# Performance work log

Measured on AMD Instinct MI355X. Metric: run time of the kernel, lower is better.

## Reference

```python
import jax, jax.numpy as jnp
import numpy as np

NC, NPR, E, B = 200000, 100000, 500000, 200000
DIN, HID, HEADS = 16, 256, 8
D = HID // HEADS
NCOLOR, NSIZE, NGROUP = 1000, 30, 50


def setup_inputs() -> dict:
    key = jax.random.key(0)
    ks = jax.random.split(key, 24)
    g = lambda i, shape, s=0.05: jax.random.normal(ks[i], shape, jnp.float32) * s
    return dict(
        customer_x=g(0, (NC, DIN), 1.0),
        product_x=g(1, (NPR, DIN), 1.0),
        proj_cust_W=g(2, (DIN, HID)), proj_cust_b=jnp.zeros((HID,), jnp.float32),
        proj_prod_W=g(3, (DIN, HID)), proj_prod_b=jnp.zeros((HID,), jnp.float32),
        att_src_r=g(4, (HEADS, D)), att_dst_r=g(5, (HEADS, D)),
        att_src_rb=g(6, (HEADS, D)), att_dst_rb=g(7, (HEADS, D)),
        q_sem=g(8, (HID,)), k_lin_W=g(9, (HID, HID)), k_lin_b=jnp.zeros((HID,), jnp.float32),
        color_emb=g(10, (NCOLOR, 8), 1.0),
        size_emb=g(11, (NSIZE, 4), 1.0),
        group_emb=g(12, (NGROUP, 4), 1.0),
        fc1_W=g(13, (HID * 2 + 16, 128)), fc1_b=jnp.zeros((128,), jnp.float32),
        fc2_W=g(14, (128, 32)), fc2_b=jnp.zeros((32,), jnp.float32),
        fc3_W=g(15, (32, 1)), fc3_b=jnp.zeros((1,), jnp.float32),
        bn1_gamma=jnp.ones((128,), jnp.float32), bn1_beta=jnp.zeros((128,), jnp.float32),
        bn2_gamma=jnp.ones((32,), jnp.float32), bn2_beta=jnp.zeros((32,), jnp.float32),
        edge_src=jax.random.randint(ks[16], (E,), 0, NC),
        edge_dst=jax.random.randint(ks[17], (E,), 0, NPR),
        label_src=jax.random.randint(ks[18], (B,), 0, NC),
        label_dst=jax.random.randint(ks[19], (B,), 0, NPR),
        size_idx=jax.random.randint(ks[20], (B,), 0, NSIZE),
        color_idx=jax.random.randint(ks[21], (B,), 0, NCOLOR),
        group_idx=jax.random.randint(ks[22], (B,), 0, NGROUP),
    )


def _edge_softmax(logits, dst, n):
    # destination-grouped softmax over edges; logits: [E,H]
    m = jax.ops.segment_max(logits, dst, num_segments=n)
    m = jnp.where(jnp.isfinite(m), m, 0.0)
    e = jnp.exp(logits - m[dst])
    s = jax.ops.segment_sum(e, dst, num_segments=n)
    return e / (s[dst] + 1e-16)


def _han_relation(h_src, h_dst, a_src, a_dst, src, dst, n_dst):
    # h_*: [N,H,D]; a_*: [H,D]
    logits = (h_src * a_src).sum(-1)[src] + (h_dst * a_dst).sum(-1)[dst]  # [E,H]
    logits = jax.nn.leaky_relu(logits, 0.2)
    alpha = _edge_softmax(logits, dst, n_dst)
    msg = alpha[:, :, None] * h_src[src]  # [E,H,D]
    out = jax.ops.segment_sum(msg, dst, num_segments=n_dst)
    return jax.nn.relu(out.reshape(n_dst, -1))  # [N_dst, H*D]


def _group(outs, q, kW, kb):
    # semantic attention over metapaths (PyG HANConv group)
    stk = jnp.stack(outs)  # [M,N,F]
    score = (q * jnp.tanh(stk @ kW + kb).mean(1)).sum(-1)  # [M]
    attn = jax.nn.softmax(score)
    return jnp.einsum('m,mnf->nf', attn, stk)


def _bn(x, gamma, beta):
    mu = x.mean(0)
    var = x.var(0)
    return (x - mu) * jax.lax.rsqrt(var + 1e-5) * gamma + beta


def reference(customer_x, product_x, proj_cust_W, proj_cust_b, proj_prod_W, proj_prod_b,
              att_src_r, att_dst_r, att_src_rb, att_dst_rb, q_sem, k_lin_W, k_lin_b,
              color_emb, size_emb, group_emb, fc1_W, fc1_b, fc2_W, fc2_b, fc3_W, fc3_b,
              bn1_gamma, bn1_beta, bn2_gamma, bn2_beta,
              edge_src, edge_dst, label_src, label_dst, size_idx, color_idx, group_idx):
    h_c = (customer_x @ proj_cust_W + proj_cust_b).reshape(-1, HEADS, D)
    h_p = (product_x @ proj_prod_W + proj_prod_b).reshape(-1, HEADS, D)
    # relation customer -returns-> product
    out_p = _han_relation(h_c, h_p, att_src_r, att_dst_r, edge_src, edge_dst, NPR)
    # relation product -returned_by-> customer (reversed edges)
    out_c = _han_relation(h_p, h_c, att_src_rb, att_dst_rb, edge_dst, edge_src, NC)
    cust = _group([out_c], q_sem, k_lin_W, k_lin_b)  # [NC, 256]
    prod = _group([out_p], q_sem, k_lin_W, k_lin_b)  # [NPR, 256]
    feat = jnp.concatenate([cust[label_src], prod[label_dst],
                            size_emb[size_idx], color_emb[color_idx], group_emb[group_idx]], axis=-1)
    x = jax.nn.relu(feat @ fc1_W + fc1_b)
    x = _bn(x, bn1_gamma, bn1_beta)
    x = jax.nn.relu(x @ fc2_W + fc2_b)
    x = _bn(x, bn2_gamma, bn2_beta)
    return x @ fc3_W + fc3_b
```

## Files before the change

### kernel.cpp

```cpp
#include <hip/hip_runtime.h>

#define NCC 200000
#define NPRR 100000
#define NEE 500000
#define NBB 200000
#define CAPP 96000
#define CAPC 160000

typedef __attribute__((ext_vector_type(8))) short bf16x8;
typedef __attribute__((ext_vector_type(16))) float f32x16;

__device__ __forceinline__ float b2f(unsigned short u){ return __uint_as_float(((unsigned)u)<<16); }
__device__ __forceinline__ unsigned short f2b(float f){
  unsigned x = __float_as_uint(f);
  return (unsigned short)((x + 0x7fffu + ((x>>16)&1u)) >> 16);
}


__global__ __launch_bounds__(256) void wa_prep2(
    const float* __restrict__ Wc, const float* __restrict__ bc,
    const float* __restrict__ attAc, const float* __restrict__ attBc,
    const float* __restrict__ Wp, const float* __restrict__ bp,
    const float* __restrict__ attAp, const float* __restrict__ attBp,
    float* __restrict__ WAc, float* __restrict__ WAp)
{
  int tid = threadIdx.x;
  for (int task = tid; task < 4*17*8; task += 256) {
    int grp = task / 136, rem = task % 136;
    int k = rem >> 3, h = rem & 7;
    const float* att = (grp==0)?attAc:(grp==1)?attBc:(grp==2)?attAp:attBp;
    const float* W   = (grp<2)?Wc:Wp;
    const float* bias= (grp<2)?bc:bp;
    const float* row = (k < 16) ? (W + k*256) : bias;
    float acc = 0.f;
    for (int d = 0; d < 32; d++) acc = fmaf(row[h*32+d], att[h*32+d], acc);
    if (grp<2) WAc[(grp&1)*136 + rem] = acc;
    else       WAp[(grp&1)*136 + rem] = acc;
  }
}

__global__ __launch_bounds__(256) void prep_proj(
    const float* __restrict__ Wc, const float* __restrict__ Wp,
    const float* __restrict__ WAc, const float* __restrict__ WAp,
    unsigned short* __restrict__ WtC, unsigned short* __restrict__ WtP,
    unsigned short* __restrict__ WAtC, unsigned short* __restrict__ WAtP)
{
  int idx = blockIdx.x*256 + threadIdx.x;
  if (idx < 4096){ int n=idx>>4, k=idx&15; WtC[idx]=f2b(Wc[k*256+n]); }
  else if (idx < 8192){ int t=idx-4096; int n=t>>4, k=t&15; WtP[t]=f2b(Wp[k*256+n]); }
  else if (idx < 8704){ int t=idx-8192; int n=t>>4, k=t&15;
    WAtC[t] = (n<16)? f2b(WAc[(n>>3)*136 + k*8 + (n&7)]) : (unsigned short)0; }
  else if (idx < 9216){ int t=idx-8704; int n=t>>4, k=t&15;
    WAtP[t] = (n<16)? f2b(WAp[(n>>3)*136 + k*8 + (n&7)]) : (unsigned short)0; }
}

__global__ __launch_bounds__(256) void prep_fc1(const float* __restrict__ fc1W,
    const float* __restrict__ fc1b,
    const float* __restrict__ size_emb, const float* __restrict__ color_emb,
    const float* __restrict__ group_emb,
    unsigned short* __restrict__ BtC, unsigned short* __restrict__ BtP,
    float* __restrict__ Ts, float* __restrict__ Tc, float* __restrict__ Tg)
{
  int idx = blockIdx.x*256 + threadIdx.x;
  if (idx < 32768){
    int n = idx>>8, k = idx&255;
    BtC[idx] = f2b(fc1W[k*128 + n]);
  } else if (idx < 65536){
    int t = idx - 32768;
    int n = t>>8, k = t&255;
    BtP[t] = f2b(fc1W[(256+k)*128 + n]);
  } else if (idx < 65536 + 30*128){
    int t = idx - 65536;
    int s = t>>7, j = t&127;
    float a = fc1b[j];
    #pragma unroll
    for (int c=0;c<4;c++) a = fmaf(size_emb[s*4+c], fc1W[(512+c)*128+j], a);
    Ts[t] = a;
  } else if (idx < 65536 + 30*128 + 1000*128){
    int t = idx - 65536 - 30*128;
    int col = t>>7, j = t&127;
    float a = 0.f;
    #pragma unroll
    for (int c=0;c<8;c++) a = fmaf(color_emb[col*8+c], fc1W[(516+c)*128+j], a);
    Tc[t] = a;
  } else if (idx < 65536 + 30*128 + 1000*128 + 50*128){
    int t = idx - 65536 - 30*128 - 1000*128;
    int g = t>>7, j = t&127;
    float a = 0.f;
    #pragma unroll
    for (int c=0;c<4;c++) a = fmaf(group_emb[g*4+c], fc1W[(524+c)*128+j], a);
    Tg[t] = a;
  }
}

#define PROJ_NB 2048
__global__ __launch_bounds__(256) void proj_hist(const float* __restrict__ X,
    const unsigned short* __restrict__ Wt, const unsigned short* __restrict__ WAt,
    const float* __restrict__ WA,
    unsigned short* __restrict__ H, float* __restrict__ sA, float* __restrict__ sB,
    int nt, int nHist,
    const int* __restrict__ src, const int* __restrict__ dst,
    int* __restrict__ cnt_c, int* __restrict__ cnt_p, int E,
    int* __restrict__ rank_r, int* __restrict__ rank_rb,
    const int* __restrict__ lsrc, const int* __restrict__ ldst,
    int* __restrict__ used_c, int* __restrict__ used_p, int B)
{
  __shared__ unsigned short wt[4608];
  __shared__ float biasS[16];
  int tid = threadIdx.x;
  int bid = blockIdx.x;
  int both = 2*nHist;
  bool isHist; int rid;
  if (bid < both){ isHist = (bid & 1); rid = bid >> 1; }
  else           { isHist = false;    rid = nHist + (bid - both); }
  if (isHist){
    int e = rid*256 + tid;
    if (e < E){
      rank_r [e] = atomicAdd(&cnt_p[dst[e]], 1);
      rank_rb[e] = atomicAdd(&cnt_c[src[e]], 1);
    }
    if (e < B){
      used_c[lsrc[e]] = 1;
      used_p[ldst[e]] = 1;
    }
    return;
  }
  for (int i=tid; i<512; i+=256) ((uint4*)wt)[i] = ((const uint4*)Wt)[i];
  for (int i=tid; i<64;  i+=256) ((uint4*)(wt+4096))[i] = ((const uint4*)WAt)[i];
  if (tid < 16) biasS[tid] = WA[(tid>>3)*136 + 128 + (tid&7)];
  __syncthreads();
  int wv = tid>>6, lane = tid&63, m = lane&31, hi = lane>>5;
  for (int t = rid; t < nt; t += PROJ_NB){
    int node = t*32 + m;
    bf16x8 a;
    {
      const float4* xr = (const float4*)(X + (long long)node*16 + hi*8);
      float4 f0 = xr[0], f1 = xr[1];
      unsigned short av[8] = {f2b(f0.x),f2b(f0.y),f2b(f0.z),f2b(f0.w),
                              f2b(f1.x),f2b(f1.y),f2b(f1.z),f2b(f1.w)};
      a = *(bf16x8*)av;
    }
    #pragma unroll
    for (int s=0;s<2;s++){
      int c0 = wv*64 + s*32;
      bf16x8 b = *(const bf16x8*)(wt + (c0+m)*16 + hi*8);
      f32x16 acc;
      #pragma unroll
      for (int i=0;i<16;i++) acc[i]=0.f;
      acc = __builtin_amdgcn_mfma_f32_32x32x16_bf16(a, b, acc, 0, 0, 0);
      #pragma unroll
      for (int reg=0; reg<16; reg++){
        int row = (reg&3) + 8*(reg>>2) + 4*hi;
        H[(long long)(t*32+row)*256 + c0 + m] = f2b(acc[reg]);
      }
    }
    if (wv == 0){
      bf16x8 b = *(const bf16x8*)(wt + 4096 + m*16 + hi*8);
      f32x16 acc;
      #pragma unroll
      for (int i=0;i<16;i++) acc[i]=0.f;
      acc = __builtin_amdgcn_mfma_f32_32x32x16_bf16(a, b, acc, 0, 0, 0);
      if (m < 16){
        float bias = biasS[m];
        float* dst2 = (m < 8) ? sA : sB;
        int h = m & 7;
        #pragma unroll
        for (int reg=0; reg<16; reg++){
          int row = (reg&3) + 8*(reg>>2) + 4*hi;
          dst2[(long long)(t*32+row)*8 + h] = acc[reg] + bias;
        }
      }
    }
  }
}

__global__ __launch_bounds__(256) void scan_p1f(const int* __restrict__ cnt_p, int* __restrict__ bsum_p, int Np,
    const int* __restrict__ cnt_c, int* __restrict__ bsum_c, int Nc, int BP, int BC,
    const int* __restrict__ used_p, const int* __restrict__ used_c, int* __restrict__ L, int nComp)
{
  __shared__ int red[256];
  __shared__ int hcnt[16];
  int tid = threadIdx.x;
  int bid = blockIdx.x;
  if (bid >= BP + BC){
    int blk2 = bid - (BP + BC);
    int n = blk2*256 + tid;
    if (tid < 16) hcnt[tid] = 0;
    __syncthreads();
    if (n < Np && used_p[n]){
      int b = min((cnt_p[n]+3)>>2, 7);
      atomicAdd(&hcnt[b], 1);
    }
    if (n < Nc && used_c[n]){
      int b = min((cnt_c[n]+3)>>2, 7);
      atomicAdd(&hcnt[8+b], 1);
    }
    __syncthreads();
    if (tid < 8       && hcnt[tid])  atomicAdd(&L[8+tid],      hcnt[tid]);
    else if (tid < 16 && hcnt[tid])  atomicAdd(&L[16+(tid-8)], hcnt[tid]);
    return;
  }
  const int* cnt; int* bsum; int N; int blk;
  if (bid < BP){ cnt=cnt_p; bsum=bsum_p; N=Np; blk=bid; }
  else         { cnt=cnt_c; bsum=bsum_c; N=Nc; blk=bid-BP; }
  int base = blk*1024 + tid*4;
  int s = 0;
  #pragma unroll
  for (int k=0;k<4;k++){ int i=base+k; if (i<N) s += cnt[i]; }
  red[tid] = s;
  __syncthreads();
  for (int off=128; off>0; off>>=1){ if (tid<off) red[tid]+=red[tid+off]; __syncthreads(); }
  if (tid==0) bsum[blk] = red[0];
}

__global__ __launch_bounds__(256) void scan_p2f(int* __restrict__ bsum_p, int Bp, int* __restrict__ rowptr_p, int Np,
    int* __restrict__ bsum_c, int Bc, int* __restrict__ rowptr_c, int Nc, int* __restrict__ L)
{
  __shared__ int ts[256];
  int tid = threadIdx.x;
  if (blockIdx.x == 2){
    if (tid == 0){
      int s = 0;
      #pragma unroll
      for (int b=0;b<8;b++){ L[24+b] = s; s += L[8+b]; }
      L[0] = s;
      s = 0;
      #pragma unroll
      for (int b=0;b<8;b++){ L[32+b] = s; s += L[16+b]; }
      L[1] = s;
    }
    return;
  }
  int* bsum; int B; int* rowptr; int N;
  if (blockIdx.x == 0){ bsum=bsum_p; B=Bp; rowptr=rowptr_p; N=Np; }
  else                { bsum=bsum_c; B=Bc; rowptr=rowptr_c; N=Nc; }
  int v = (tid<B) ? bsum[tid] : 0;
  ts[tid] = v;
  __syncthreads();
  for (int off=1; off<256; off<<=1){
    int t = (tid>=off) ? ts[tid-off] : 0;
    __syncthreads();
    ts[tid] += t;
    __syncthreads();
  }
  if (tid < B) bsum[tid] = ts[tid] - v;
  if (tid == B-1) rowptr[N] = ts[tid];
}

__global__ __launch_bounds__(256) void scan_p3f(const int* __restrict__ cnt_p, const int* __restrict__ bsum_p,
    int* __restrict__ rowptr_p, int Np,
    const int* __restrict__ cnt_c, const int* __restrict__ bsum_c,
    int* __restrict__ rowptr_c, int Nc, int BP)
{
  __shared__ int ts[256];
  const int* cnt; const int* bsum; int* rowptr; int N; int blk;
  if ((int)blockIdx.x < BP){ cnt=cnt_p; bsum=bsum_p; rowptr=rowptr_p; N=Np; blk=blockIdx.x; }
  else                     { cnt=cnt_c; bsum=bsum_c; rowptr=rowptr_c; N=Nc; blk=blockIdx.x-BP; }
  int tid = threadIdx.x;
  int base = blk*1024 + tid*4;
  int v[4]; int s = 0;
  #pragma unroll
  for (int k=0;k<4;k++){ int i=base+k; v[k] = (i<N) ? cnt[i] : 0; s += v[k]; }
  ts[tid] = s;
  __syncthreads();
  for (int off=1; off<256; off<<=1){
    int t = (tid>=off) ? ts[tid-off] : 0;
    __syncthreads();
    ts[tid] += t;
    __syncthreads();
  }
  int run = bsum[blk] + ts[tid] - s;
  #pragma unroll
  for (int k=0;k<4;k++){ int i=base+k; if (i<N){ rowptr[i]=run; run += v[k]; } }
}

__global__ __launch_bounds__(256) void mega2(
    const int* __restrict__ src, const int* __restrict__ dst,
    const int* __restrict__ rp_r, const int* __restrict__ rp_rb,
    const int* __restrict__ rank_r, const int* __restrict__ rank_rb,
    int* __restrict__ si_r, int* __restrict__ si_rb, int E,
    const int* __restrict__ used_p, const int* __restrict__ rowptr_p, int Np,
    int4* __restrict__ list_p, int* __restrict__ L, int* __restrict__ smap_p,
    const int* __restrict__ used_c, const int* __restrict__ rowptr_c, int Nc,
    int4* __restrict__ list_c, int* __restrict__ smap_c,
    int nComp,
    const float* __restrict__ X, const unsigned short* __restrict__ Wt,
    const unsigned short* __restrict__ WAt, const float* __restrict__ WA,
    unsigned short* __restrict__ H, float* __restrict__ sA, float* __restrict__ sB,
    int nt, int nProj)
{
  __shared__ unsigned short wt[4608];
  __shared__ float biasS[16];
  __shared__ int hcnt[16];
  __shared__ int hbase[16];
  __shared__ int hcur[16];
  int tid = threadIdx.x, bid = blockIdx.x;
  int nB = nComp + nProj;
  int both = 2*nB;
  bool isB; int rid;
  if (bid < both){ isB = (bid & 1); rid = bid >> 1; }
  else           { isB = false;     rid = nB + (bid - both); }
  if (isB){
    if (rid < nComp){
      int n = rid*256 + tid;
      if (tid < 16){ hcnt[tid] = 0; hcur[tid] = 0; }
      __syncthreads();
      int bp = -1, bc = -1;
      int e0p=0,e1p=0,e0c=0,e1c=0;
      if (n < Np && used_p[n]){
        e0p = rowptr_p[n]; e1p = rowptr_p[n+1];
        bp = min(((e1p-e0p)+3)>>2, 7);
        atomicAdd(&hcnt[bp], 1);
      }
      if (n < Nc && used_c[n]){
        e0c = rowptr_c[n]; e1c = rowptr_c[n+1];
        bc = min(((e1c-e0c)+3)>>2, 7);
        atomicAdd(&hcnt[8+bc], 1);
      }
      __syncthreads();
      if (tid < 8)        hbase[tid] = hcnt[tid] ? atomicAdd(&L[64+tid],     hcnt[tid]) : 0;
      else if (tid < 16)  hbase[tid] = hcnt[tid] ? atomicAdd(&L[72+(tid-8)], hcnt[tid]) : 0;
      __syncthreads();
      if (bp >= 0){
        int r = atomicAdd(&hcur[bp], 1);
        int slot = L[24+bp] + hbase[bp] + r;
        if (slot < CAPP){ list_p[slot] = make_int4(n, e0p, e1p, 0); smap_p[n] = slot; }
      }
      if (bc >= 0){
        int r = atomicAdd(&hcur[8+bc], 1);
        int slot = L[32+bc] + hbase[8+bc] + r;
        if (slot < CAPC){ list_c[slot] = make_int4(n, e0c, e1c, 0); smap_c[n] = slot; }
      }
      return;
    }
    int pid = rid - nComp;
    for (int i=tid; i<512; i+=256) ((uint4*)wt)[i] = ((const uint4*)Wt)[i];
    for (int i=tid; i<64;  i+=256) ((uint4*)(wt+4096))[i] = ((const uint4*)WAt)[i];
    if (tid < 16) biasS[tid] = WA[(tid>>3)*136 + 128 + (tid&7)];
    __syncthreads();
    int wv = tid>>6, lane = tid&63, m = lane&31, hi = lane>>5;
    for (int t = pid; t < nt; t += nProj){
      int node = t*32 + m;
      bf16x8 a;
      {
        const float4* xr = (const float4*)(X + (long long)node*16 + hi*8);
        float4 f0 = xr[0], f1 = xr[1];
        unsigned short av[8] = {f2b(f0.x),f2b(f0.y),f2b(f0.z),f2b(f0.w),
                                f2b(f1.x),f2b(f1.y),f2b(f1.z),f2b(f1.w)};
        a = *(bf16x8*)av;
      }
      #pragma unroll
      for (int s=0;s<2;s++){
        int c0 = wv*64 + s*32;
        bf16x8 b = *(const bf16x8*)(wt + (c0+m)*16 + hi*8);
        f32x16 acc;
        #pragma unroll
        for (int i=0;i<16;i++) acc[i]=0.f;
        acc = __builtin_amdgcn_mfma_f32_32x32x16_bf16(a, b, acc, 0, 0, 0);
        #pragma unroll
        for (int reg=0; reg<16; reg++){
          int row = (reg&3) + 8*(reg>>2) + 4*hi;
          H[(long long)(t*32+row)*256 + c0 + m] = f2b(acc[reg]);
        }
      }
      if (wv == 0){
        bf16x8 b = *(const bf16x8*)(wt + 4096 + m*16 + hi*8);
        f32x16 acc;
        #pragma unroll
        for (int i=0;i<16;i++) acc[i]=0.f;
        acc = __builtin_amdgcn_mfma_f32_32x32x16_bf16(a, b, acc, 0, 0, 0);
        if (m < 16){
          float bias = biasS[m];
          float* dst2 = (m < 8) ? sA : sB;
          int h = m & 7;
          #pragma unroll
          for (int reg=0; reg<16; reg++){
            int row = (reg&3) + 8*(reg>>2) + 4*hi;
            dst2[(long long)(t*32+row)*8 + h] = acc[reg] + bias;
          }
        }
      }
    }
    return;
  }
  int e = rid*256 + tid;
  if (e < E){
    int s = src[e], d = dst[e];
    si_r [rp_r [d] + rank_r [e]] = s;
    si_rb[rp_rb[s] + rank_rb[e]] = d;
  }
}

__device__ __forceinline__ void agg_block(
    const int4* __restrict__ list, int cnt, int base,
    const int* __restrict__ srcidx,
    const float* __restrict__ sSrc, const float* __restrict__ sDst,
    const unsigned short* __restrict__ H, const unsigned short* __restrict__ Bt,
    unsigned short* __restrict__ Y, int tid, unsigned short* feat)
{
  int wv = tid>>6, lane = tid&63;
  int g = lane>>4, ln = lane&15, h = ln>>1;
  #pragma unroll
  for (int t=0;t<2;t++){
    int r = wv*8 + t*4 + g;
    int slot = base + r;
    float acc[16];
    #pragma unroll
    for (int c=0;c<16;c++) acc[c]=0.f;
    float den = 0.f;
    int node = -1, e0 = 0, e1 = 0;
    if (slot < cnt){
      int4 L = list[slot];
      node = L.x; e0 = L.y; e1 = L.z;
    }
    if (node >= 0 && e1 > e0){
      int elast = e1 - 1;
      float sdh = sDst[(long long)node*8 + h];
      for (int e = e0; e < e1; e += 4){
        int i1 = min(e+1, elast), i2 = min(e+2, elast), i3 = min(e+3, elast);
        int s0 = srcidx[e],  s1 = srcidx[i1];
        int s2 = srcidx[i2], s3 = srcidx[i3];
        const uint4* p0 = (const uint4*)&H[(long long)s0*256 + ln*16];
        const uint4* p1 = (const uint4*)&H[(long long)s1*256 + ln*16];
        const uint4* p2 = (const uint4*)&H[(long long)s2*256 + ln*16];
        const uint4* p3 = (const uint4*)&H[(long long)s3*256 + ln*16];
        uint4 uA0 = p0[0], uA1 = p0[1];
        uint4 uB0 = p1[0], uB1 = p1[1];
        uint4 uC0 = p2[0], uC1 = p2[1];
        uint4 uD0 = p3[0], uD1 = p3[1];
        float l0 = sSrc[(long long)s0*8 + h];
        float l1 = sSrc[(long long)s1*8 + h];
        float l2 = sSrc[(long long)s2*8 + h];
        float l3 = sSrc[(long long)s3*8 + h];
        l0 += sdh; l1 += sdh; l2 += sdh; l3 += sdh;
        float w0 = __expf(l0 > 0.f ? l0 : 0.2f*l0);
        float w1 = (e+1 < e1) ? __expf(l1 > 0.f ? l1 : 0.2f*l1) : 0.f;
        float w2 = (e+2 < e1) ? __expf(l2 > 0.f ? l2 : 0.2f*l2) : 0.f;
        float w3 = (e+3 < e1) ? __expf(l3 > 0.f ? l3 : 0.2f*l3) : 0.f;
        den += (w0 + w1) + (w2 + w3);
        unsigned ua[8] = {uA0.x,uA0.y,uA0.z,uA0.w, uA1.x,uA1.y,uA1.z,uA1.w};
        unsigned ub[8] = {uB0.x,uB0.y,uB0.z,uB0.w, uB1.x,uB1.y,uB1.z,uB1.w};
        unsigned uc[8] = {uC0.x,uC0.y,uC0.z,uC0.w, uC1.x,uC1.y,uC1.z,uC1.w};
        unsigned ud[8] = {uD0.x,uD0.y,uD0.z,uD0.w, uD1.x,uD1.y,uD1.z,uD1.w};
        #pragma unroll
        for (int p=0;p<8;p++){
          acc[p*2]   = fmaf(w0, b2f((unsigned short)(ua[p]&0xffffu)), acc[p*2]);
          acc[p*2+1] = fmaf(w0, b2f((unsigned short)(ua[p]>>16)),     acc[p*2+1]);
          acc[p*2]   = fmaf(w1, b2f((unsigned short)(ub[p]&0xffffu)), acc[p*2]);
          acc[p*2+1] = fmaf(w1, b2f((unsigned short)(ub[p]>>16)),     acc[p*2+1]);
          acc[p*2]   = fmaf(w2, b2f((unsigned short)(uc[p]&0xffffu)), acc[p*2]);
          acc[p*2+1] = fmaf(w2, b2f((unsigned short)(uc[p]>>16)),     acc[p*2+1]);
          acc[p*2]   = fmaf(w3, b2f((unsigned short)(ud[p]&0xffffu)), acc[p*2]);
          acc[p*2+1] = fmaf(w3, b2f((unsigned short)(ud[p]>>16)),     acc[p*2+1]);
        }
      }
    }
    float inv = 1.f/(den + 1e-16f);
    unsigned short ov[16];
    #pragma unroll
    for (int c=0;c<16;c++) ov[c] = f2b(fmaxf(acc[c]*inv, 0.f));
    *(uint4*)&feat[r*264 + ln*16]     = *(uint4*)&ov[0];
    *(uint4*)&feat[r*264 + ln*16 + 8] = *(uint4*)&ov[8];
  }
  __syncthreads();
  int m = lane&31, hi = lane>>5;
  f32x16 acc;
  #pragma unroll
  for (int i=0;i<16;i++) acc[i]=0.f;
  const unsigned short* ap  = feat + m*264 + hi*8;
  const unsigned short* btp = Bt + (wv*32 + m)*256 + hi*8;
  #pragma unroll 4
  for (int ks=0; ks<16; ks++){
    bf16x8 a = *(const bf16x8*)(ap + ks*16);
    bf16x8 b = *(const bf16x8*)(btp + ks*16);
    acc = __builtin_amdgcn_mfma_f32_32x32x16_bf16(a, b, acc, 0, 0, 0);
  }
  int col = wv*32 + m;
  #pragma unroll
  for (int reg=0; reg<16; reg++){
    int row = (reg&3) + 8*(reg>>2) + 4*hi;
    Y[(long long)(base+row)*128 + col] = f2b(acc[reg]);
  }
}

__global__ __launch_bounds__(256) void agg2(
    const int4* __restrict__ listP, const int* __restrict__ lcntP,
    const int* __restrict__ siR,
    const float* __restrict__ sCr, const float* __restrict__ sPr,
    const unsigned short* __restrict__ Hc, const unsigned short* __restrict__ BtP,
    unsigned short* __restrict__ YP, int nP,
    const int4* __restrict__ listC, const int* __restrict__ lcntC,
    const int* __restrict__ siRB,
    const float* __restrict__ sPrb, const float* __restrict__ sCrb,
    const unsigned short* __restrict__ Hp, const unsigned short* __restrict__ BtC,
    unsigned short* __restrict__ YC)
{
  __shared__ unsigned short feat[32*264];
  int bid = blockIdx.x, tid = threadIdx.x;
  int both = 2*nP;
  bool isR; int rid;
  if (bid < both){ isR = !(bid & 1); rid = bid >> 1; }
  else           { isR = false;      rid = nP + (bid - both); }
  if (isR){
    int cnt = *lcntP;
    int base = rid*32;
    if (base >= cnt) return;
    agg_block(listP, cnt, base, siR, sCr, sPr, Hc, BtP, YP, tid, feat);
  } else {
    int cnt = *lcntC;
    int base = rid*32;
    if (base >= cnt) return;
    agg_block(listC, cnt, base, siRB, sPrb, sCrb, Hp, BtC, YC, tid, feat);
  }
}

__global__ __launch_bounds__(256) void gather_fc1(
    const unsigned short* __restrict__ Yc, const unsigned short* __restrict__ Yp,
    const int* __restrict__ smap_c, const int* __restrict__ smap_p,
    const float* __restrict__ Ts, const float* __restrict__ Tc, const float* __restrict__ Tg,
    const int* __restrict__ lsrc, const int* __restrict__ ldst,
    const int* __restrict__ sidx, const int* __restrict__ cidx, const int* __restrict__ gidx,
    unsigned short* __restrict__ x1, float* __restrict__ bnsum, int ntiles)
{
  __shared__ float redS[16][128];
  __shared__ float redQ[16][128];
  int tid = threadIdx.x;
  int rl = tid>>4, g = tid&15;
  float sacc[8] = {0,0,0,0,0,0,0,0};
  float qacc[8] = {0,0,0,0,0,0,0,0};
  for (int t = blockIdx.x; t < ntiles; t += gridDim.x){
    long long row = (long long)t*16 + rl;
    int ls = smap_c[lsrc[row]], ld = smap_p[ldst[row]];
    int si = sidx[row], ci = cidx[row], gi = gidx[row];
    uint4 uc = *(const uint4*)&Yc[(long long)ls*128 + g*8];
    uint4 up = *(const uint4*)&Yp[(long long)ld*128 + g*8];
    float4 t0 = *(const float4*)&Ts[si*128 + g*8];
    float4 t1 = *(const float4*)&Ts[si*128 + g*8 + 4];
    float4 c0 = *(const float4*)&Tc[ci*128 + g*8];
    float4 c1 = *(const float4*)&Tc[ci*128 + g*8 + 4];
    float4 g0 = *(const float4*)&Tg[gi*128 + g*8];
    float4 g1 = *(const float4*)&Tg[gi*128 + g*8 + 4];
    unsigned ucs[4] = {uc.x,uc.y,uc.z,uc.w};
    unsigned ups[4] = {up.x,up.y,up.z,up.w};
    float tb[8] = {t0.x+c0.x+g0.x, t0.y+c0.y+g0.y, t0.z+c0.z+g0.z, t0.w+c0.w+g0.w,
                   t1.x+c1.x+g1.x, t1.y+c1.y+g1.y, t1.z+c1.z+g1.z, t1.w+c1.w+g1.w};
    unsigned short ov[8];
    #pragma unroll
    for (int p=0;p<4;p++){
      float vl = b2f((unsigned short)(ucs[p]&0xffffu)) + b2f((unsigned short)(ups[p]&0xffffu)) + tb[p*2];
      float vh = b2f((unsigned short)(ucs[p]>>16))     + b2f((unsigned short)(ups[p]>>16))     + tb[p*2+1];
      vl = fmaxf(vl, 0.f); vh = fmaxf(vh, 0.f);
      ov[p*2] = f2b(vl); ov[p*2+1] = f2b(vh);
      sacc[p*2]   += vl; qacc[p*2]   += vl*vl;
      sacc[p*2+1] += vh; qacc[p*2+1] += vh*vh;
    }
    *(uint4*)&x1[row*128 + g*8] = *(uint4*)ov;
  }
  #pragma unroll
  for (int j=0;j<8;j++){ redS[rl][g*8+j]=sacc[j]; redQ[rl][g*8+j]=qacc[j]; }
  __syncthreads();
  if (tid < 128){
    float s=0.f, q=0.f;
    #pragma unroll
    for (int r=0;r<16;r++){ s += redS[r][tid]; q += redQ[r][tid]; }
    atomicAdd(&bnsum[tid], s);
    atomicAdd(&bnsum[128+tid], q);
  }
}

__global__ void bn1_fold(const float* __restrict__ bnsum,
    const float* __restrict__ gamma, const float* __restrict__ beta,
    const float* __restrict__ fc2W, const float* __restrict__ fc2b,
    unsigned short* __restrict__ Bt2, float* __restrict__ b2p, float invB)
{
  __shared__ float sc[128], sh[128];
  int tid = threadIdx.x;
  if (tid<128){
    float mu  = bnsum[tid]*invB;
    float var = bnsum[128+tid]*invB - mu*mu;
    float s = gamma[tid] * rsqrtf(var + 1e-5f);
    sc[tid]=s; sh[tid]= beta[tid] - mu*s;
  }
  __syncthreads();
  for (int idx=tid; idx<32*128; idx+=256){
    int n = idx>>7, k = idx&127;
    Bt2[idx] = f2b(sc[k]*fc2W[k*32+n]);
  }
  if (tid<32){
    float a = fc2b[tid];
    for (int k=0;k<128;k++) a = fmaf(sh[k], fc2W[k*32+tid], a);
    b2p[tid]=a;
  }
}

__global__ __launch_bounds__(256) void fc2_mfma(const unsigned short* __restrict__ x1,
    const unsigned short* __restrict__ Bt2, const float* __restrict__ b2p,
    unsigned short* __restrict__ x2, float* __restrict__ bnsum2, int M)
{
  __shared__ unsigned short xt[128*136];
  __shared__ unsigned short wt[32*136];
  __shared__ float redS[4][32];
  __shared__ float redQ[4][32];
  int tid = threadIdx.x;
  long long base = (long long)blockIdx.x*128;
  for (int idx=tid; idx<128*16; idx+=256){
    int r = idx>>4, c = idx&15;
    uint4 u = make_uint4(0,0,0,0);
    if (base + r < M) u = *(const uint4*)&x1[(base+r)*128 + c*8];
    *(uint4*)&xt[r*136 + c*8] = u;
  }
  for (int idx=tid; idx<32*16; idx+=256){
    int r = idx>>4, c = idx&15;
    *(uint4*)&wt[r*136 + c*8] = *(const uint4*)&Bt2[r*128 + c*8];
  }
  __syncthreads();
  int wv = tid>>6, lane = tid&63;
  int m = lane&31, hi = lane>>5;
  f32x16 acc;
  #pragma unroll
  for (int i=0;i<16;i++) acc[i]=0.f;
  const unsigned short* ap = xt + (wv*32 + m)*136 + hi*8;
  const unsigned short* bp = wt + m*136 + hi*8;
  #pragma unroll
  for (int ks=0; ks<8; ks++){
    bf16x8 a = *(const bf16x8*)(ap + ks*16);
    bf16x8 b = *(const bf16x8*)(bp + ks*16);
    acc = __builtin_amdgcn_mfma_f32_32x32x16_bf16(a, b, acc, 0, 0, 0);
  }
  int col = m;
  float bias = b2p[col];
  float s=0.f, q=0.f;
  #pragma unroll
  for (int reg=0; reg<16; reg++){
    int row = (reg&3) + 8*(reg>>2) + 4*hi;
    long long grow = base + wv*32 + row;
    float v = fmaxf(acc[reg] + bias, 0.f);
    if (grow < M) x2[grow*32 + col] = f2b(v);
    s += v; q += v*v;
  }
  if (base + 128 > M){
    s = 0.f; q = 0.f;
    #pragma unroll
    for (int reg=0; reg<16; reg++){
      int row = (reg&3) + 8*(reg>>2) + 4*hi;
      long long grow = base + wv*32 + row;
      float v = fmaxf(acc[reg] + bias, 0.f);
      if (grow < M){ s += v; q += v*v; }
    }
  }
  s += __shfl_xor(s, 32);
  q += __shfl_xor(q, 32);
  if (hi == 0){ redS[wv][col] = s; redQ[wv][col] = q; }
  __syncthreads();
  if (tid < 32){
    float a = redS[0][tid]+redS[1][tid]+redS[2][tid]+redS[3][tid];
    float b = redQ[0][tid]+redQ[1][tid]+redQ[2][tid]+redQ[3][tid];
    atomicAdd(&bnsum2[tid], a);
    atomicAdd(&bnsum2[32+tid], b);
  }
}

__global__ void bn2_fold(const float* __restrict__ bnsum2,
    const float* __restrict__ gamma2, const float* __restrict__ beta2,
    const float* __restrict__ fc3W, const float* __restrict__ fc3b,
    float* __restrict__ w3p, float invB)
{
  __shared__ float sh3[32];
  int tid = threadIdx.x;
  if (tid<32){
    float mu  = bnsum2[tid]*invB;
    float var = bnsum2[32+tid]*invB - mu*mu;
    float s   = gamma2[tid] * rsqrtf(var + 1e-5f);
    float shv = beta2[tid] - mu*s;
    float w   = fc3W[tid];
    w3p[tid]  = s*w;
    sh3[tid]  = shv*w;
  }
  __syncthreads();
  if (tid==0){
    float a = fc3b[0];
    for (int j=0;j<32;j++) a += sh3[j];
    w3p[32] = a;
  }
}

__global__ __launch_bounds__(256) void fc3_kernel(const unsigned short* __restrict__ x2,
    const float* __restrict__ w3p, float* __restrict__ out)
{
  __shared__ float wl[34];
  int tid = threadIdx.x;
  if (tid<33) wl[tid]=w3p[tid];
  __syncthreads();
  long long row = (long long)blockIdx.x*32 + (tid>>3);
  int j0 = (tid&7)*4;
  uint2 u = *(const uint2*)(x2 + row*32 + j0);
  float a = b2f((unsigned short)(u.x&0xffffu))*wl[j0]
          + b2f((unsigned short)(u.x>>16))   *wl[j0+1]
          + b2f((unsigned short)(u.y&0xffffu))*wl[j0+2]
          + b2f((unsigned short)(u.y>>16))   *wl[j0+3];
  a += __shfl_xor(a,1);
  a += __shfl_xor(a,2);
  a += __shfl_xor(a,4);
  if ((tid&7)==0) out[row] = a + wl[32];
}

extern "C" void kernel_launch(void* const* d_in, const int* in_sizes, int n_in,
                              void* d_out, int out_size, void* d_ws, size_t ws_size,
                              hipStream_t stream)
{
  (void)in_sizes; (void)n_in; (void)out_size; (void)ws_size;
  const float* customer_x = (const float*)d_in[0];
  const float* product_x  = (const float*)d_in[1];
  const float* pcW = (const float*)d_in[2];
  const float* pcB = (const float*)d_in[3];
  const float* ppW = (const float*)d_in[4];
  const float* ppB = (const float*)d_in[5];
  const float* att_src_r  = (const float*)d_in[6];
  const float* att_dst_r  = (const float*)d_in[7];
  const float* att_src_rb = (const float*)d_in[8];
  const float* att_dst_rb = (const float*)d_in[9];
  const float* color_emb = (const float*)d_in[13];
  const float* size_emb  = (const float*)d_in[14];
  const float* group_emb = (const float*)d_in[15];
  const float* fc1W = (const float*)d_in[16];
  const float* fc1b = (const float*)d_in[17];
  const float* fc2W = (const float*)d_in[18];
  const float* fc2b = (const float*)d_in[19];
  const float* fc3W = (const float*)d_in[20];
  const float* fc3b = (const float*)d_in[21];
  const float* bn1g = (const float*)d_in[22];
  const float* bn1b = (const float*)d_in[23];
  const float* bn2g = (const float*)d_in[24];
  const float* bn2b = (const float*)d_in[25];
  const int* edge_src  = (const int*)d_in[26];
  const int* edge_dst  = (const int*)d_in[27];
  const int* label_src = (const int*)d_in[28];
  const int* label_dst = (const int*)d_in[29];
  const int* size_idx  = (const int*)d_in[30];
  const int* color_idx = (const int*)d_in[31];
  const int* group_idx = (const int*)d_in[32];

  char* ws = (char*)d_ws;
  size_t off = 0;
  auto alloc = [&](size_t bytes)->char* {
    char* p = ws + off;
    off += (bytes + 255) & ~(size_t)255;
    return p;
  };
  unsigned short* H_c  = (unsigned short*)alloc((size_t)NCC*256*2);
  unsigned short* H_p  = (unsigned short*)alloc((size_t)NPRR*256*2);
  unsigned short* Y_p  = (unsigned short*)alloc((size_t)CAPP*128*2);
  unsigned short* Y_c  = (unsigned short*)alloc((size_t)CAPC*128*2);
  float* s_cr     = (float*)alloc((size_t)NCC*8*4);
  float* s_crb    = (float*)alloc((size_t)NCC*8*4);
  float* s_pr     = (float*)alloc((size_t)NPRR*8*4);
  float* s_prb    = (float*)alloc((size_t)NPRR*8*4);
  int* rowptr_r   = (int*)alloc((size_t)(NPRR+1)*4);
  int* rowptr_rb  = (int*)alloc((size_t)(NCC+1)*4);
  int* srcidx_r   = (int*)alloc((size_t)NEE*4);
  int* srcidx_rb  = (int*)alloc((size_t)NEE*4);
  int* rank_r     = (int*)alloc((size_t)NEE*4);
  int* rank_rb    = (int*)alloc((size_t)NEE*4);
  int* cnts       = (int*)alloc((size_t)(NCC+NPRR)*2*4);
  int* cnt_c      = cnts;
  int* cnt_p      = cnts + NCC;
  int* used_c     = cnts + NCC + NPRR;
  int* used_p     = used_c + NCC;
  int* smap_p     = (int*)alloc((size_t)NPRR*4);
  int* smap_c     = (int*)alloc((size_t)NCC*4);
  int* bsum_c     = (int*)alloc(256*4);
  int* bsum_p     = (int*)alloc(256*4);
  int4* list_p    = (int4*)alloc((size_t)CAPP*16);
  int4* list_c    = (int4*)alloc((size_t)CAPC*16);
  int* lcnt       = (int*)alloc(512);
  unsigned short* BtC = (unsigned short*)alloc(128*256*2);
  unsigned short* BtP = (unsigned short*)alloc(128*256*2);
  float* Ts     = (float*)alloc(30*128*4);
  float* Tc     = (float*)alloc(1000*128*4);
  float* Tg     = (float*)alloc(50*128*4);
  float* wa_c   = (float*)alloc(272*4);
  float* wa_p   = (float*)alloc(272*4);
  unsigned short* WtC  = (unsigned short*)alloc(256*16*2);
  unsigned short* WtP  = (unsigned short*)alloc(256*16*2);
  unsigned short* WAtC = (unsigned short*)alloc(32*16*2);
  unsigned short* WAtP = (unsigned short*)alloc(32*16*2);
  float* bnsum1 = (float*)alloc(256*4);
  float* bnsum2 = (float*)alloc(64*4);
  unsigned short* Bt2 = (unsigned short*)alloc(32*128*2);
  float* b2p    = (float*)alloc(32*4);
  float* w3p    = (float*)alloc(34*4);
  unsigned short* x1b = H_p;
  unsigned short* x2b = (unsigned short*)s_cr;

  hipMemsetAsync(bnsum1, 0, 1280, stream);
  hipMemsetAsync(cnts, 0, (size_t)(NCC+NPRR)*2*4, stream);
  hipMemsetAsync(lcnt, 0, 512, stream);

  wa_prep2<<<1,256,0,stream>>>(pcW, pcB, att_src_r, att_dst_rb,
                               ppW, ppB, att_dst_r, att_src_rb, wa_c, wa_p);
  prep_proj<<<36,256,0,stream>>>(pcW, ppW, wa_c, wa_p, WtC, WtP, WAtC, WAtP);
  prep_fc1<<<(203776+255)/256,256,0,stream>>>(fc1W, fc1b, size_emb, color_emb, group_emb,
      BtC, BtP, Ts, Tc, Tg);

  const int eg = (NEE+255)/256;
  const int BP = (NPRR+1023)/1024;
  const int BC = (NCC +1023)/1024;
  const int nComp = (NCC+255)/256;
  const int nProjP = 1024;
  const int nP = CAPP/32;
  const int nC = CAPC/32;

  proj_hist<<<PROJ_NB+eg,256,0,stream>>>(customer_x, WtC, WAtC, wa_c,
      H_c, s_cr, s_crb, NCC/32, eg,
      edge_src, edge_dst, cnt_c, cnt_p, NEE, rank_r, rank_rb,
      label_src, label_dst, used_c, used_p, NBB);

  scan_p1f<<<BP+BC+nComp,256,0,stream>>>(cnt_p, bsum_p, NPRR, cnt_c, bsum_c, NCC, BP, BC,
      used_p, used_c, lcnt, nComp);
  scan_p2f<<<3,256,0,stream>>>(bsum_p, BP, rowptr_r, NPRR, bsum_c, BC, rowptr_rb, NCC, lcnt);
  scan_p3f<<<BP+BC,256,0,stream>>>(cnt_p, bsum_p, rowptr_r, NPRR,
      cnt_c, bsum_c, rowptr_rb, NCC, BP);

  mega2<<<eg + (nComp+nProjP),256,0,stream>>>(edge_src, edge_dst,
      rowptr_r, rowptr_rb, rank_r, rank_rb, srcidx_r, srcidx_rb, NEE,
      used_p, rowptr_r, NPRR, list_p, lcnt, smap_p,
      used_c, rowptr_rb, NCC, list_c, smap_c, nComp,
      product_x, WtP, WAtP, wa_p, H_p, s_pr, s_prb, NPRR/32, nProjP);

  agg2<<<nP+nC,256,0,stream>>>(list_p, &lcnt[0], srcidx_r, s_cr, s_pr, H_c, BtP, Y_p, nP,
                               list_c, &lcnt[1], srcidx_rb, s_prb, s_crb, H_p, BtC, Y_c);

  gather_fc1<<<2048,256,0,stream>>>(Y_c, Y_p, smap_c, smap_p, Ts, Tc, Tg,
      label_src, label_dst, size_idx, color_idx, group_idx, x1b, bnsum1, NBB/16);

  bn1_fold<<<1,256,0,stream>>>(bnsum1, bn1g, bn1b, fc2W, fc2b, Bt2, b2p, 1.0f/NBB);
  fc2_mfma<<<(NBB+127)/128,256,0,stream>>>(x1b, Bt2, b2p, x2b, bnsum2, NBB);
  bn2_fold<<<1,64,0,stream>>>(bnsum2, bn2g, bn2b, fc3W, fc3b, w3p, 1.0f/NBB);
  fc3_kernel<<<NBB/32,256,0,stream>>>(x2b, w3p, (float*)d_out);
}
```

Before: 514.9 us.

## Split edge histogram across prep and projection kernels; precompute label slot indices

The atomic edge histogram is split at a fixed edge index. The first half, plus the label 'used' marking, is interleaved into the fc1 weight-prep kernel, so that latency-bound atomic work overlaps the prep work. The second half stays in the projection kernel. The agg2 launch gains extra blocks that resolve the label-to-slot double indirection once, so gather_fc1 reads the slots directly instead of chasing two dependent loads. This adds a kernel argument set and two small buffers, and the block interleaving may shift load balance.

```diff
diff --git a/kernel.cpp b/kernel.cpp
--- a/kernel.cpp
+++ b/kernel.cpp
@@ -6,6 +6,7 @@
 #define NBB 200000
 #define CAPP 96000
 #define CAPC 160000
+#define E2SPLIT 250112
 
 typedef __attribute__((ext_vector_type(8))) short bf16x8;
 typedef __attribute__((ext_vector_type(16))) float f32x16;
@@ -54,14 +55,36 @@
     WAtP[t] = (n<16)? f2b(WAp[(n>>3)*136 + k*8 + (n&7)]) : (unsigned short)0; }
 }
 
-__global__ __launch_bounds__(256) void prep_fc1(const float* __restrict__ fc1W,
+__global__ __launch_bounds__(256) void prep_fc1h(const float* __restrict__ fc1W,
     const float* __restrict__ fc1b,
     const float* __restrict__ size_emb, const float* __restrict__ color_emb,
     const float* __restrict__ group_emb,
     unsigned short* __restrict__ BtC, unsigned short* __restrict__ BtP,
-    float* __restrict__ Ts, float* __restrict__ Tc, float* __restrict__ Tg)
-{
-  int idx = blockIdx.x*256 + threadIdx.x;
+    float* __restrict__ Ts, float* __restrict__ Tc, float* __restrict__ Tg,
+    int nPrep,
+    const int* __restrict__ src, const int* __restrict__ dst,
+    int* __restrict__ cnt_c, int* __restrict__ cnt_p,
+    int* __restrict__ rank_r, int* __restrict__ rank_rb, int E2,
+    const int* __restrict__ lsrc, const int* __restrict__ ldst,
+    int* __restrict__ used_c, int* __restrict__ used_p, int B)
+{
+  int bid = blockIdx.x, tid = threadIdx.x;
+  bool isHist; int rid;
+  if (bid < 2*nPrep){ isHist = (bid & 1); rid = bid >> 1; }
+  else              { isHist = true;     rid = nPrep + (bid - 2*nPrep); }
+  if (isHist){
+    int e = rid*256 + tid;
+    if (e < E2){
+      rank_r [e] = atomicAdd(&cnt_p[dst[e]], 1);
+      rank_rb[e] = atomicAdd(&cnt_c[src[e]], 1);
+    }
+    if (e < B){
+      used_c[lsrc[e]] = 1;
+      used_p[ldst[e]] = 1;
+    }
+    return;
+  }
+  int idx = rid*256 + tid;
   if (idx < 32768){
     int n = idx>>8, k = idx&255;
     BtC[idx] = f2b(fc1W[k*128 + n]);
@@ -100,10 +123,8 @@
     unsigned short* __restrict__ H, float* __restrict__ sA, float* __restrict__ sB,
     int nt, int nHist,
     const int* __restrict__ src, const int* __restrict__ dst,
-    int* __restrict__ cnt_c, int* __restrict__ cnt_p, int E,
-    int* __restrict__ rank_r, int* __restrict__ rank_rb,
-    const int* __restrict__ lsrc, const int* __restrict__ ldst,
-    int* __restrict__ used_c, int* __restrict__ used_p, int B)
+    int* __restrict__ cnt_c, int* __restrict__ cnt_p, int E, int E2,
+    int* __restrict__ rank_r, int* __restrict__ rank_rb)
 {
   __shared__ unsigned short wt[4608];
   __shared__ float biasS[16];
@@ -114,14 +135,10 @@
   if (bid < both){ isHist = (bid & 1); rid = bid >> 1; }
   else           { isHist = false;    rid = nHist + (bid - both); }
   if (isHist){
-    int e = rid*256 + tid;
+    int e = E2 + rid*256 + tid;
     if (e < E){
       rank_r [e] = atomicAdd(&cnt_p[dst[e]], 1);
       rank_rb[e] = atomicAdd(&cnt_c[src[e]], 1);
-    }
-    if (e < B){
-      used_c[lsrc[e]] = 1;
-      used_p[ldst[e]] = 1;
     }
     return;
   }
@@ -493,14 +510,28 @@
     const int* __restrict__ siRB,
     const float* __restrict__ sPrb, const float* __restrict__ sCrb,
     const unsigned short* __restrict__ Hp, const unsigned short* __restrict__ BtC,
-    unsigned short* __restrict__ YC)
+    unsigned short* __restrict__ YC,
+    const int* __restrict__ lsrc, const int* __restrict__ ldst,
+    const int* __restrict__ smap_c, const int* __restrict__ smap_p,
+    int* __restrict__ lslot, int* __restrict__ ldslot, int B, int nT)
 {
   __shared__ unsigned short feat[32*264];
   int bid = blockIdx.x, tid = threadIdx.x;
+  bool isT = false; int idx;
+  if (bid < 2*nT){ if (bid & 1){ isT = true; } idx = bid >> 1; }
+  else            { idx = bid - nT; }
+  if (isT){
+    int row = idx*256 + tid;
+    if (row < B){
+      lslot [row] = smap_c[lsrc[row]];
+      ldslot[row] = smap_p[ldst[row]];
+    }
+    return;
+  }
   int both = 2*nP;
   bool isR; int rid;
-  if (bid < both){ isR = !(bid & 1); rid = bid >> 1; }
-  else           { isR = false;      rid = nP + (bid - both); }
+  if (idx < both){ isR = !(idx & 1); rid = idx >> 1; }
+  else           { isR = false;      rid = nP + (idx - both); }
   if (isR){
     int cnt = *lcntP;
     int base = rid*32;
@@ -516,9 +547,8 @@
 
 __global__ __launch_bounds__(256) void gather_fc1(
     const unsigned short* __restrict__ Yc, const unsigned short* __restrict__ Yp,
-    const int* __restrict__ smap_c, const int* __restrict__ smap_p,
+    const int* __restrict__ lslot, const int* __restrict__ ldslot,
     const float* __restrict__ Ts, const float* __restrict__ Tc, const float* __restrict__ Tg,
-    const int* __restrict__ lsrc, const int* __restrict__ ldst,
     const int* __restrict__ sidx, const int* __restrict__ cidx, const int* __restrict__ gidx,
     unsigned short* __restrict__ x1, float* __restrict__ bnsum, int ntiles)
 {
@@ -530,7 +560,7 @@
   float qacc[8] = {0,0,0,0,0,0,0,0};
   for (int t = blockIdx.x; t < ntiles; t += gridDim.x){
     long long row = (long long)t*16 + rl;
-    int ls = smap_c[lsrc[row]], ld = smap_p[ldst[row]];
+    int ls = lslot[row], ld = ldslot[row];
     int si = sidx[row], ci = cidx[row], gi = gidx[row];
     uint4 uc = *(const uint4*)&Yc[(long long)ls*128 + g*8];
     uint4 up = *(const uint4*)&Yp[(long long)ld*128 + g*8];
@@ -768,6 +798,8 @@
   int* used_p     = used_c + NCC;
   int* smap_p     = (int*)alloc((size_t)NPRR*4);
   int* smap_c     = (int*)alloc((size_t)NCC*4);
+  int* lslot      = (int*)alloc((size_t)NBB*4);
+  int* ldslot     = (int*)alloc((size_t)NBB*4);
   int* bsum_c     = (int*)alloc(256*4);
   int* bsum_p     = (int*)alloc(256*4);
   int4* list_p    = (int4*)alloc((size_t)CAPP*16);
@@ -796,12 +828,6 @@
   hipMemsetAsync(cnts, 0, (size_t)(NCC+NPRR)*2*4, stream);
   hipMemsetAsync(lcnt, 0, 512, stream);
 
-  wa_prep2<<<1,256,0,stream>>>(pcW, pcB, att_src_r, att_dst_rb,
-                               ppW, ppB, att_dst_r, att_src_rb, wa_c, wa_p);
-  prep_proj<<<36,256,0,stream>>>(pcW, ppW, wa_c, wa_p, WtC, WtP, WAtC, WAtP);
-  prep_fc1<<<(203776+255)/256,256,0,stream>>>(fc1W, fc1b, size_emb, color_emb, group_emb,
-      BtC, BtP, Ts, Tc, Tg);
-
   const int eg = (NEE+255)/256;
   const int BP = (NPRR+1023)/1024;
   const int BC = (NCC +1023)/1024;
@@ -809,11 +835,22 @@
   const int nProjP = 1024;
   const int nP = CAPP/32;
   const int nC = CAPC/32;
-
-  proj_hist<<<PROJ_NB+eg,256,0,stream>>>(customer_x, WtC, WAtC, wa_c,
-      H_c, s_cr, s_crb, NCC/32, eg,
-      edge_src, edge_dst, cnt_c, cnt_p, NEE, rank_r, rank_rb,
+  const int nT = (NBB+255)/256;
+  const int nPrep = 796;
+  const int nHistA = E2SPLIT/256;
+  const int nHistB = (NEE - E2SPLIT + 255)/256;
+
+  wa_prep2<<<1,256,0,stream>>>(pcW, pcB, att_src_r, att_dst_rb,
+                               ppW, ppB, att_dst_r, att_src_rb, wa_c, wa_p);
+  prep_proj<<<36,256,0,stream>>>(pcW, ppW, wa_c, wa_p, WtC, WtP, WAtC, WAtP);
+  prep_fc1h<<<nPrep+nHistA,256,0,stream>>>(fc1W, fc1b, size_emb, color_emb, group_emb,
+      BtC, BtP, Ts, Tc, Tg, nPrep,
+      edge_src, edge_dst, cnt_c, cnt_p, rank_r, rank_rb, E2SPLIT,
       label_src, label_dst, used_c, used_p, NBB);
+
+  proj_hist<<<PROJ_NB+nHistB,256,0,stream>>>(customer_x, WtC, WAtC, wa_c,
+      H_c, s_cr, s_crb, NCC/32, nHistB,
+      edge_src, edge_dst, cnt_c, cnt_p, NEE, E2SPLIT, rank_r, rank_rb);
 
   scan_p1f<<<BP+BC+nComp,256,0,stream>>>(cnt_p, bsum_p, NPRR, cnt_c, bsum_c, NCC, BP, BC,
       used_p, used_c, lcnt, nComp);
@@ -827,11 +864,12 @@
       used_c, rowptr_rb, NCC, list_c, smap_c, nComp,
       product_x, WtP, WAtP, wa_p, H_p, s_pr, s_prb, NPRR/32, nProjP);
 
-  agg2<<<nP+nC,256,0,stream>>>(list_p, &lcnt[0], srcidx_r, s_cr, s_pr, H_c, BtP, Y_p, nP,
-                               list_c, &lcnt[1], srcidx_rb, s_prb, s_crb, H_p, BtC, Y_c);
-
-  gather_fc1<<<2048,256,0,stream>>>(Y_c, Y_p, smap_c, smap_p, Ts, Tc, Tg,
-      label_src, label_dst, size_idx, color_idx, group_idx, x1b, bnsum1, NBB/16);
+  agg2<<<nT+nP+nC,256,0,stream>>>(list_p, &lcnt[0], srcidx_r, s_cr, s_pr, H_c, BtP, Y_p, nP,
+                               list_c, &lcnt[1], srcidx_rb, s_prb, s_crb, H_p, BtC, Y_c,
+                               label_src, label_dst, smap_c, smap_p, lslot, ldslot, NBB, nT);
+
+  gather_fc1<<<2048,256,0,stream>>>(Y_c, Y_p, lslot, ldslot, Ts, Tc, Tg,
+      size_idx, color_idx, group_idx, x1b, bnsum1, NBB/16);
 
   bn1_fold<<<1,256,0,stream>>>(bnsum1, bn1g, bn1b, fc2W, fc2b, Bt2, b2p, 1.0f/NBB);
   fc2_mfma<<<(NBB+127)/128,256,0,stream>>>(x1b, Bt2, b2p, x2b, bnsum2, NBB);
```

Result: slower. 526.1 us (+2.2%).
